# Kernel optimization log

Hardware: AMD Instinct MI355X
Metric: run time of the kernel (lower is better)

The kernel has to match this reference:

```python
import jax, jax.numpy as jnp
import numpy as np

TEMPERATURE = 0.8
TOP_P = 0.9
NEG_INF = float('-inf')


def _top_k_filter(logits, k):
    # keep only the top-k logits per row; mask the rest to -inf.
    # torch.topk + scatter mask == threshold at the k-th largest value (ties measure-zero for float logits)
    kth = jax.lax.top_k(logits, k)[0][..., -1:]  # [B, 1]
    return jnp.where(logits < kth, NEG_INF, logits)


def _top_p_filter(logits, p):
    # nucleus filtering: sort desc, cumulative softmax mass, drop tail past p (always keep the top token)
    B, V = logits.shape
    order = jnp.argsort(-logits, axis=-1)                       # [B, V] descending order
    sorted_logits = jnp.take_along_axis(logits, order, axis=-1)
    cdf = jnp.cumsum(jax.nn.softmax(sorted_logits, axis=-1), axis=-1)
    remove_sorted = cdf > p
    remove_sorted = jnp.roll(remove_sorted, 1, axis=-1).at[..., 0].set(False)  # shift so first token crossing p is kept
    rows = jnp.arange(B)[:, None]
    remove = jnp.zeros((B, V), dtype=bool).at[rows, order].set(remove_sorted)  # scatter back to original positions
    return jnp.where(remove, NEG_INF, logits)


def _sample_multinomial(probs, key):
    # inverse-CDF sampling: idx = #{cumsum <= r}
    r = jax.random.uniform(key, (probs.shape[0], 1), dtype=probs.dtype)
    cdf = jnp.cumsum(probs, axis=-1)
    return jnp.sum(cdf <= r, axis=-1, keepdims=True)  # [B, 1] int


def setup_inputs() -> dict:
    key = jax.random.key(0)
    logits = jax.random.normal(key, (256, 50257), dtype=jnp.float32) * 4.0
    return {"logits": logits, "top_k": 50}


def reference(logits, top_k):
    logits = logits / TEMPERATURE
    logits = _top_k_filter(logits, top_k)
    logits = _top_p_filter(logits, TOP_P)
    probs = jax.nn.softmax(logits, axis=-1)
    next_ids = _sample_multinomial(probs, jax.random.fold_in(jax.random.key(0), 1))
    return next_ids
```

## Files before the change

kernel.cpp:

```cpp
#include <hip/hip_runtime.h>
#include <stdint.h>


#define S_CHUNKS 8
#define PB       256
#define SEG      128
#define TB       256
#define CAPN     1024
#define WCAP     256
#define TOPP     0.9f
#define TOPT_F   10.0f
#define OK10     0xC1200000u

__device__ __forceinline__ unsigned orderKey(float x) {
  unsigned u = __float_as_uint(x);
  return (u & 0x80000000u) ? ~u : (u | 0x80000000u);
}

__device__ __forceinline__ void threefry2x32(unsigned k0, unsigned k1,
                                             unsigned x0, unsigned x1,
                                             unsigned &o0, unsigned &o1) {
  unsigned k2 = k0 ^ k1 ^ 0x1BD11BDAu;
  x0 += k0; x1 += k1;
#define TFR(rr) { x0 += x1; x1 = (x1 << (rr)) | (x1 >> (32 - (rr))); x1 ^= x0; }
  TFR(13) TFR(15) TFR(26) TFR(6)
  x0 += k1; x1 += k2 + 1u;
  TFR(17) TFR(29) TFR(16) TFR(24)
  x0 += k2; x1 += k0 + 2u;
  TFR(13) TFR(15) TFR(26) TFR(6)
  x0 += k0; x1 += k1 + 3u;
  TFR(17) TFR(29) TFR(16) TFR(24)
  x0 += k1; x1 += k2 + 4u;
  TFR(13) TFR(15) TFR(26) TFR(6)
  x0 += k2; x1 += k0 + 5u;
#undef TFR
  o0 = x0; o1 = x1;
}

__global__ __launch_bounds__(PB) void k_pass1(
    const float* __restrict__ logits, int* __restrict__ scnt,
    uint2* __restrict__ seg, int V) {
  __shared__ unsigned lcnt;

  const int row = blockIdx.y, chunk = blockIdx.x, tid = threadIdx.x;
  const float* __restrict__ rp = logits + (size_t)row * (size_t)V;
  const float4* __restrict__ rp4 = (const float4*)rp;
  const int V4 = V >> 2;
  const int beg = (int)((long long)chunk * V4 / S_CHUNKS);
  const int end = (int)((long long)(chunk + 1) * V4 / S_CHUNKS);
  const bool last = (chunk == S_CHUNKS - 1);
  const int rembeg = V4 << 2;
  const int sb = row * S_CHUNKS + chunk;
  uint2* __restrict__ op = seg + (size_t)sb * SEG;

  if (tid == 0) lcnt = 0u;
  __syncthreads();

#define EMIT(xv, xi) do { float _x = (xv);                               \
    if (_x >= TOPT_F) { unsigned _p = atomicAdd(&lcnt, 1u);              \
      if (_p < SEG) op[_p] = make_uint2(__float_as_uint(_x), (unsigned)(xi)); \
    } } while (0)

  for (int i = beg + tid; i < end; i += PB) {
    float4 v = rp4[i];
    EMIT(v.x, (i << 2));     EMIT(v.y, (i << 2) + 1);
    EMIT(v.z, (i << 2) + 2); EMIT(v.w, (i << 2) + 3);
  }
  if (last)
    for (int i = rembeg + tid; i < V; i += PB) EMIT(rp[i], i);
#undef EMIT
  __syncthreads();
  if (tid == 0) scnt[sb] = (lcnt > (unsigned)SEG) ? -1 : (int)lcnt;
}

__global__ __launch_bounds__(TB) void k_tail(
    const float* __restrict__ logits, const int* __restrict__ scnt,
    const uint2* __restrict__ seg, const int* __restrict__ topk_ptr,
    int* __restrict__ out, int V) {
  __shared__ float    candv[CAPN];
  __shared__ int      candi[CAPN];
  __shared__ unsigned hist2[TB];
  __shared__ float    wv[WCAP];
  __shared__ int      wi[WCAP];
  __shared__ float    sv[WCAP];
  __shared__ int      si[WCAP];
  __shared__ float    evl[WCAP];
  __shared__ short    ordl[WCAP];
  __shared__ int      s_off[S_CHUNKS + 1];
  __shared__ int      s_c[S_CHUNKS];
  __shared__ unsigned s_wc, s_thr;
  __shared__ int      s_n, s_bstar, s_mode, s_ns;

  const int tid = threadIdx.x, lane = tid & 63, wid = tid >> 6;
  const int row = blockIdx.x;
  const float* __restrict__ rp = logits + (size_t)row * (size_t)V;
  int k = topk_ptr[0];
  if (k < 1) k = 1;
  if (k > V) k = V;

  if (tid < S_CHUNKS) s_c[tid] = scnt[row * S_CHUNKS + tid];
  if (tid == 0) s_wc = 0u;
  __syncthreads();
  if (tid == 0) {
    int off = 0, bad = 0;
    for (int c = 0; c < S_CHUNKS; ++c) {
      int cc = s_c[c];
      if (cc < 0) { bad = 1; cc = 0; }
      s_off[c] = off;
      off += cc;
    }
    int n = bad ? -1 : off;
    if (n > CAPN) n = -1;
    s_off[S_CHUNKS] = n;
    s_mode = (n < k) ? 1 : 0;
  }
  __syncthreads();
  int n = s_off[S_CHUNKS];

  if (s_mode == 0) {
    for (int c = 0; c < S_CHUNKS; ++c) {
      const int o = s_off[c];
      const int cn = ((c + 1 < S_CHUNKS) ? s_off[c + 1] : n) - o;
      const uint2* __restrict__ gp = seg + (size_t)(row * S_CHUNKS + c) * SEG;
      for (int i = tid; i < cn; i += TB) {
        uint2 u = gp[i];
        candv[o + i] = __uint_as_float(u.x);
        candi[o + i] = (int)u.y;
      }
    }
    hist2[tid] = 0u;
    __syncthreads();
    for (int i = tid; i < n; i += TB) {
      unsigned b = (orderKey(candv[i]) - OK10) >> 16;
      if (b > 255u) b = 255u;
      atomicAdd(&hist2[b], 1u);
    }
    __syncthreads();
    if (wid == 0) {
      unsigned h0 = hist2[4 * lane],     h1 = hist2[4 * lane + 1];
      unsigned h2 = hist2[4 * lane + 2], h3 = hist2[4 * lane + 3];
      int suf = (int)(h0 + h1 + h2 + h3);
      for (int d = 1; d < 64; d <<= 1) {
        int t = __shfl_down(suf, d);
        if (lane + d < 64) suf += t;
      }
      int sufn = (lane < 63) ? __shfl_down(suf, 1) : 0;
      unsigned long long mk = __ballot(suf >= k);
      int Ls = (int)__popcll(mk) - 1;
      if (lane == Ls) {
        int cum = sufn, bs;
        if (cum + (int)h3 >= k) bs = 4 * Ls + 3;
        else { cum += (int)h3;
          if (cum + (int)h2 >= k) bs = 4 * Ls + 2;
          else { cum += (int)h2;
            bs = (cum + (int)h1 >= k) ? 4 * Ls + 1 : 4 * Ls; } }
        s_bstar = bs;
      }
    }
    __syncthreads();
    if (tid == 0) {
      int b = s_bstar;
      if (b >= 1) s_thr = OK10 + ((unsigned)b << 16) - 4u;
      else        s_mode = 1;
    }
    __syncthreads();
  }

  if (s_mode == 1) {
    unsigned lo = 1u, hi = 0xFFFFFFFFu;
    while (lo < hi) {
      unsigned mid = lo + ((hi - lo + 1u) >> 1);
      int c = 0;
      for (int i = tid; i < V; i += TB) c += (orderKey(rp[i]) >= mid);
      hist2[tid] = (unsigned)c;
      __syncthreads();
      for (int st = TB / 2; st; st >>= 1) {
        if (tid < st) hist2[tid] += hist2[tid + st];
        __syncthreads();
      }
      unsigned tot = hist2[0];
      __syncthreads();
      if ((int)tot >= k) lo = mid; else hi = mid - 1u;
    }
    if (tid == 0) { s_thr = (lo >= 5u) ? lo - 4u : 1u; s_wc = 0u; }
    __syncthreads();
    const unsigned thr = s_thr;
    for (int i = tid; i < V; i += TB) {
      float x = rp[i];
      if (orderKey(x) >= thr) {
        unsigned p = atomicAdd(&s_wc, 1u);
        if (p < CAPN) { candv[p] = x; candi[p] = i; }
      }
    }
    __syncthreads();
    if (tid == 0) {
      int nn = (int)s_wc;
      s_n = (nn > CAPN) ? CAPN : nn;
      s_wc = 0u;
    }
    __syncthreads();
    n = s_n;
  }

  {
    const unsigned thr = s_thr;
    for (int i = tid; i < n; i += TB) {
      float x = candv[i];
      if (orderKey(x) >= thr) {
        unsigned p = atomicAdd(&s_wc, 1u);
        if (p < WCAP) { wv[p] = x / 0.8f; wi[p] = candi[i]; }
      }
    }
  }
  __syncthreads();
  int m = (int)s_wc;
  if (m > WCAP) m = WCAP;
  if (m == 0) { if (tid == 0) out[row] = V; return; }

  for (int i = tid; i < m; i += TB) {
    float v = wv[i];
    int   id = wi[i];
    int   rk = 0;
    for (int j = 0; j < m; ++j) {
      float vj = wv[j];
      rk += (vj > v) || (vj == v && wi[j] < id);
    }
    sv[rk] = v;
    si[rk] = id;
  }
  __syncthreads();

  if (tid == 0) {
    const int kk = (k < m) ? k : m;
    int ns = kk;
    float kv = sv[kk - 1];
    while (ns < m && sv[ns] == kv) ++ns;
    s_ns = ns;
  }
  __syncthreads();
  const int ns = s_ns;

  if (wid != 0) return;

  unsigned tk0, tk1, o0, o1;
  threefry2x32(0u, 0u, 0u, 1u, tk0, tk1);
  threefry2x32(tk0, tk1, 0u, (unsigned)row, o0, o1);
  unsigned bits = o0 ^ o1;
  float r0 = __uint_as_float((bits >> 9) | 0x3F800000u) - 1.0f;
  const float rr = (r0 < 0.f) ? 0.f : r0;

  if (ns <= 64) {
    float myv  = (lane < ns) ? sv[lane] : 0.f;
    int   myid = (lane < ns) ? si[lane] : 0x7FFFFFFF;
    const float mx = __shfl(myv, 0);
    float mye = (lane < ns) ? expf(myv - mx) : 0.f;

    float S = 0.f;
    for (int i = 0; i < ns; ++i) S += __shfl(mye, i);
    float c = 0.f;
    int K = ns;
    for (int i = 0; i < ns; ++i) {
      if (i > 0 && c > TOPP) { K = i; break; }
      c += __shfl(mye, i) / S;
    }
    float S2 = 0.f;
    for (int i = 0; i < K; ++i) S2 += __shfl(mye, i);

    int rk = 0;
    for (int j = 0; j < K; ++j) {
      int idj = __shfl(myid, j);
      rk += (idj < myid);
    }
    float c2 = 0.f;
    int ans = V;
    for (int t = 0; t < K; ++t) {
      unsigned long long mm = __ballot((lane < K) && (rk == t));
      int src = __ffsll((unsigned long long)mm) - 1;
      c2 += __shfl(mye, src) / S2;
      if (c2 > rr) { ans = __shfl(myid, src); break; }
    }
    if (lane == 0) out[row] = ans;
    return;
  }

  for (int i = lane; i < ns; i += 64) evl[i] = expf(sv[i] - sv[0]);
  if (lane == 0) {
    float S = 0.f;
    for (int i = 0; i < ns; ++i) S += evl[i];
    float c = 0.f;
    int K = ns;
    for (int i = 0; i < ns; ++i) {
      if (i > 0 && c > TOPP) { K = i; break; }
      c += evl[i] / S;
    }
    float S2 = 0.f;
    for (int i = 0; i < K; ++i) S2 += evl[i];
    for (int i = 0; i < K; ++i) {
      int id = si[i], rk2 = 0;
      for (int j = 0; j < K; ++j) rk2 += (si[j] < id);
      ordl[rk2] = (short)i;
    }
    float c2 = 0.f;
    int ans = V;
    for (int t = 0; t < K; ++t) {
      int i = ordl[t];
      c2 += evl[i] / S2;
      if (c2 > rr) { ans = si[i]; break; }
    }
    out[row] = ans;
  }
}

extern "C" void kernel_launch(void* const* d_in, const int* in_sizes, int n_in,
                              void* d_out, int out_size, void* d_ws, size_t ws_size,
                              hipStream_t stream) {
  const float* logits = (const float*)d_in[0];
  const int*   topk   = (const int*)d_in[1];
  int*         out    = (int*)d_out;
  const int B = out_size;
  const int V = in_sizes[0] / B;

  char* ws = (char*)d_ws;
  int*   scnt = (int*)ws;
  uint2* seg  = (uint2*)(ws + (size_t)B * S_CHUNKS * 4);

  hipLaunchKernelGGL(k_pass1, dim3(S_CHUNKS, B), dim3(PB), 0, stream,
                     logits, scnt, seg, V);
  hipLaunchKernelGGL(k_tail, dim3(B), dim3(TB), 0, stream,
                     logits, scnt, seg, topk, out, V);
}
```

Measured before the change: 106.1 us.

## Fuse candidate prefilter pass into per-row tail kernel with 1024-thread blocks

```diff
diff --git a/kernel.cpp b/kernel.cpp
--- a/kernel.cpp
+++ b/kernel.cpp
@@ -2,10 +2,7 @@
 #include <stdint.h>
 
 
-#define S_CHUNKS 8
-#define PB       256
-#define SEG      128
-#define TB       256
+#define TB       1024
 #define CAPN     1024
 #define WCAP     256
 #define TOPP     0.9f
@@ -37,45 +34,8 @@
   o0 = x0; o1 = x1;
 }
 
-__global__ __launch_bounds__(PB) void k_pass1(
-    const float* __restrict__ logits, int* __restrict__ scnt,
-    uint2* __restrict__ seg, int V) {
-  __shared__ unsigned lcnt;
-
-  const int row = blockIdx.y, chunk = blockIdx.x, tid = threadIdx.x;
-  const float* __restrict__ rp = logits + (size_t)row * (size_t)V;
-  const float4* __restrict__ rp4 = (const float4*)rp;
-  const int V4 = V >> 2;
-  const int beg = (int)((long long)chunk * V4 / S_CHUNKS);
-  const int end = (int)((long long)(chunk + 1) * V4 / S_CHUNKS);
-  const bool last = (chunk == S_CHUNKS - 1);
-  const int rembeg = V4 << 2;
-  const int sb = row * S_CHUNKS + chunk;
-  uint2* __restrict__ op = seg + (size_t)sb * SEG;
-
-  if (tid == 0) lcnt = 0u;
-  __syncthreads();
-
-#define EMIT(xv, xi) do { float _x = (xv);                               \
-    if (_x >= TOPT_F) { unsigned _p = atomicAdd(&lcnt, 1u);              \
-      if (_p < SEG) op[_p] = make_uint2(__float_as_uint(_x), (unsigned)(xi)); \
-    } } while (0)
-
-  for (int i = beg + tid; i < end; i += PB) {
-    float4 v = rp4[i];
-    EMIT(v.x, (i << 2));     EMIT(v.y, (i << 2) + 1);
-    EMIT(v.z, (i << 2) + 2); EMIT(v.w, (i << 2) + 3);
-  }
-  if (last)
-    for (int i = rembeg + tid; i < V; i += PB) EMIT(rp[i], i);
-#undef EMIT
-  __syncthreads();
-  if (tid == 0) scnt[sb] = (lcnt > (unsigned)SEG) ? -1 : (int)lcnt;
-}
-
-__global__ __launch_bounds__(TB) void k_tail(
-    const float* __restrict__ logits, const int* __restrict__ scnt,
-    const uint2* __restrict__ seg, const int* __restrict__ topk_ptr,
+__global__ __launch_bounds__(TB) void k_fused(
+    const float* __restrict__ logits, const int* __restrict__ topk_ptr,
     int* __restrict__ out, int V) {
   __shared__ float    candv[CAPN];
   __shared__ int      candi[CAPN];
@@ -86,48 +46,63 @@
   __shared__ int      si[WCAP];
   __shared__ float    evl[WCAP];
   __shared__ short    ordl[WCAP];
-  __shared__ int      s_off[S_CHUNKS + 1];
-  __shared__ int      s_c[S_CHUNKS];
-  __shared__ unsigned s_wc, s_thr;
+  __shared__ unsigned s_wc, s_thr, s_cnt;
   __shared__ int      s_n, s_bstar, s_mode, s_ns;
 
   const int tid = threadIdx.x, lane = tid & 63, wid = tid >> 6;
   const int row = blockIdx.x;
   const float* __restrict__ rp = logits + (size_t)row * (size_t)V;
+  const float4* __restrict__ rp4 = (const float4*)rp;
+  const int V4 = V >> 2;
+  const int rembeg = V4 << 2;
   int k = topk_ptr[0];
   if (k < 1) k = 1;
   if (k > V) k = V;
 
-  if (tid < S_CHUNKS) s_c[tid] = scnt[row * S_CHUNKS + tid];
-  if (tid == 0) s_wc = 0u;
-  __syncthreads();
+  if (tid == 0) { s_cnt = 0u; s_wc = 0u; }
+  __syncthreads();
+
+#define EMIT(xv, xi) do { float _x = (xv);                                \
+    if (_x >= TOPT_F) { unsigned _p = atomicAdd(&s_cnt, 1u);              \
+      if (_p < CAPN) { candv[_p] = _x; candi[_p] = (int)(xi); } } } while (0)
+
+  {
+    int i = tid;
+    for (; i + 3 * TB < V4; i += 4 * TB) {
+      float4 a = rp4[i];
+      float4 b = rp4[i + TB];
+      float4 c = rp4[i + 2 * TB];
+      float4 d = rp4[i + 3 * TB];
+      EMIT(a.x, (i << 2));              EMIT(a.y, (i << 2) + 1);
+      EMIT(a.z, (i << 2) + 2);          EMIT(a.w, (i << 2) + 3);
+      EMIT(b.x, ((i + TB) << 2));       EMIT(b.y, ((i + TB) << 2) + 1);
+      EMIT(b.z, ((i + TB) << 2) + 2);   EMIT(b.w, ((i + TB) << 2) + 3);
+      EMIT(c.x, ((i + 2 * TB) << 2));   EMIT(c.y, ((i + 2 * TB) << 2) + 1);
+      EMIT(c.z, ((i + 2 * TB) << 2) + 2); EMIT(c.w, ((i + 2 * TB) << 2) + 3);
+      EMIT(d.x, ((i + 3 * TB) << 2));   EMIT(d.y, ((i + 3 * TB) << 2) + 1);
+      EMIT(d.z, ((i + 3 * TB) << 2) + 2); EMIT(d.w, ((i + 3 * TB) << 2) + 3);
+    }
+    for (; i < V4; i += TB) {
+      float4 v = rp4[i];
+      EMIT(v.x, (i << 2));     EMIT(v.y, (i << 2) + 1);
+      EMIT(v.z, (i << 2) + 2); EMIT(v.w, (i << 2) + 3);
+    }
+    for (int j = rembeg + tid; j < V; j += TB) EMIT(rp[j], j);
+  }
+#undef EMIT
+  __syncthreads();
+
   if (tid == 0) {
-    int off = 0, bad = 0;
-    for (int c = 0; c < S_CHUNKS; ++c) {
-      int cc = s_c[c];
-      if (cc < 0) { bad = 1; cc = 0; }
-      s_off[c] = off;
-      off += cc;
-    }
-    int n = bad ? -1 : off;
-    if (n > CAPN) n = -1;
-    s_off[S_CHUNKS] = n;
-    s_mode = (n < k) ? 1 : 0;
-  }
-  __syncthreads();
-  int n = s_off[S_CHUNKS];
+    int raw = (int)s_cnt;
+    int nn = (raw > CAPN) ? -1 : raw;
+    if (nn < k) nn = -1;
+    s_n = nn;
+    s_mode = (nn < 0) ? 1 : 0;
+  }
+  __syncthreads();
+  int n = s_n;
 
   if (s_mode == 0) {
-    for (int c = 0; c < S_CHUNKS; ++c) {
-      const int o = s_off[c];
-      const int cn = ((c + 1 < S_CHUNKS) ? s_off[c + 1] : n) - o;
-      const uint2* __restrict__ gp = seg + (size_t)(row * S_CHUNKS + c) * SEG;
-      for (int i = tid; i < cn; i += TB) {
-        uint2 u = gp[i];
-        candv[o + i] = __uint_as_float(u.x);
-        candi[o + i] = (int)u.y;
-      }
-    }
     hist2[tid] = 0u;
     __syncthreads();
     for (int i = tid; i < n; i += TB) {
@@ -319,13 +294,8 @@
   int*         out    = (int*)d_out;
   const int B = out_size;
   const int V = in_sizes[0] / B;
-
-  char* ws = (char*)d_ws;
-  int*   scnt = (int*)ws;
-  uint2* seg  = (uint2*)(ws + (size_t)B * S_CHUNKS * 4);
-
-  hipLaunchKernelGGL(k_pass1, dim3(S_CHUNKS, B), dim3(PB), 0, stream,
-                     logits, scnt, seg, V);
-  hipLaunchKernelGGL(k_tail, dim3(B), dim3(TB), 0, stream,
-                     logits, scnt, seg, topk, out, V);
+  (void)d_ws; (void)ws_size;
+
+  hipLaunchKernelGGL(k_fused, dim3(B), dim3(TB), 0, stream,
+                     logits, topk, out, V);
 }
```

New measurement: 100.2 us. 1.06x faster.
